# Kernel optimization log

Hardware: AMD Instinct MI355X
Metric: run time of the kernel (lower is better)

The kernel has to match this reference:

```python
import jax, jax.numpy as jnp
import numpy as np


def setup_inputs() -> dict:
    key = jax.random.key(0)
    k1, k2, k3 = jax.random.split(key, 3)
    B, T, E = 4, 2048, 1024
    x = jax.random.normal(k1, (B, T, E), dtype=jnp.float32)
    # torch nn.Linear weight layout: [out_features, in_features]
    w_qkv = jax.random.normal(k2, (3 * E, E), dtype=jnp.float32) * (E ** -0.5)
    w_out = jax.random.normal(k3, (E, E), dtype=jnp.float32) * (E ** -0.5)
    return {"x": x, "w_qkv": w_qkv, "w_out": w_out}


def reference(x, w_qkv, w_out):
    B, T, E = x.shape
    H = 16
    D = E // H  # head_dim
    # QKV projection (Linear, bias=False): x @ W.T -> [B,T,3E]
    qkv = jnp.einsum('bte,fe->btf', x, w_qkv)
    qkv = qkv.reshape(B, T, 3, H, D).transpose(2, 0, 3, 1, 4)  # [3,B,H,T,D]
    q, k, v = qkv[0], qkv[1], qkv[2]
    scale = 1.0 / jnp.sqrt(jnp.asarray(D, dtype=x.dtype))
    att = jnp.einsum('bhqd,bhkd->bhqk', q, k) * scale  # [B,H,T,T]
    causal = jnp.tril(jnp.ones((T, T), dtype=bool))
    att = jnp.where(causal[None, None], att, jnp.asarray(-jnp.inf, dtype=att.dtype))
    att = jax.nn.softmax(att, axis=-1)
    # dropout = 0.0 (eval-mode): identity
    y = jnp.einsum('bhqk,bhkd->bhqd', att, v)  # [B,H,T,D]
    y = y.transpose(0, 2, 1, 3).reshape(B, T, E)
    return jnp.einsum('bte,fe->btf', y, w_out)
```

## Files before the change

### kernel.cpp

```cpp
#include <hip/hip_runtime.h>

typedef __bf16 bf16x8 __attribute__((ext_vector_type(8)));
typedef __bf16 bf16x4 __attribute__((ext_vector_type(4)));
typedef __bf16 bf16x2 __attribute__((ext_vector_type(2)));
typedef float f32x4 __attribute__((ext_vector_type(4)));
typedef float f32x16 __attribute__((ext_vector_type(16)));
typedef unsigned short ushortx8 __attribute__((ext_vector_type(8)));
typedef unsigned short ushortx4 __attribute__((ext_vector_type(4)));
typedef unsigned int uint32x4v __attribute__((ext_vector_type(4)));

#define DEVI static __device__ __forceinline__

DEVI unsigned short f2bf(float f) {
  unsigned int u = __builtin_bit_cast(unsigned int, f);
  u += 0x7FFFu + ((u >> 16) & 1u);
  return (unsigned short)(u >> 16);
}

DEVI bf16x8 ld8(const unsigned short* p) {
  return __builtin_bit_cast(bf16x8, *(const ushortx8*)p);
}

DEVI void gll16(const unsigned short* g, unsigned short* l) {
  __builtin_amdgcn_global_load_lds((const __attribute__((address_space(1))) void*)g,
                                   (__attribute__((address_space(3))) void*)l, 16, 0, 0);
}

#define MFMA16(a, b, c) __builtin_amdgcn_mfma_f32_16x16x32_bf16(a, b, c, 0, 0, 0)
#define MFMA32(a, b, c) __builtin_amdgcn_mfma_f32_32x32x16_bf16(a, b, c, 0, 0, 0)

DEVI unsigned pkbf(float lo, float hi) {
  bf16x2 v;
  v[0] = (__bf16)lo;
  v[1] = (__bf16)hi;
  return __builtin_bit_cast(unsigned, v);
}

DEVI float swaphalf_max(float x) {
  unsigned xu = __builtin_bit_cast(unsigned, x);
  auto pr = __builtin_amdgcn_permlane32_swap(xu, xu, false, false);
  return fmaxf(__builtin_bit_cast(float, (unsigned)pr[0]),
               __builtin_bit_cast(float, (unsigned)pr[1]));
}

DEVI float swaphalf_add(float x) {
  unsigned xu = __builtin_bit_cast(unsigned, x);
  auto pr = __builtin_amdgcn_permlane32_swap(xu, xu, false, false);
  return __builtin_bit_cast(float, (unsigned)pr[0]) +
         __builtin_bit_cast(float, (unsigned)pr[1]);
}

DEVI bf16x8 ldswz(const unsigned short* L, int row, int colsh) {
  return ld8(L + row * 64 + ((((colsh * 2) ^ ((row & 7) << 4))) >> 1));
}

#define SB 4
#define ST 2048
#define SE 1024
#define SH 16
#define SD 64
#define QSCALE 0.18033688011112042f
#define DMTHR 11.541560327111708f

__global__ void cvt_f32_bf16(const float* __restrict__ in, unsigned short* __restrict__ out, int n4) {
  int i = blockIdx.x * blockDim.x + threadIdx.x;
  if (i >= n4) return;
  float4 v = ((const float4*)in)[i];
  ushortx4 o;
  o.x = f2bf(v.x); o.y = f2bf(v.y); o.z = f2bf(v.z); o.w = f2bf(v.w);
  ((ushortx4*)out)[i] = o;
}

template<int EPI>
__global__ __launch_bounds__(256, 2) void gemm_nt(
    const unsigned short* __restrict__ A, const unsigned short* __restrict__ Bw,
    float* __restrict__ Cf,
    unsigned short* __restrict__ Qo, unsigned short* __restrict__ Ko,
    unsigned short* __restrict__ VTo,
    int M, int N, int K) {
  __shared__ unsigned short As[2][128 * 64];
  __shared__ unsigned short Bs[2][128 * 64];
  const int tid = threadIdx.x;
  const int lane = tid & 63;
  const int w = tid >> 6;
  const int wr = w >> 1, wc = w & 1;
  const int r16 = lane & 15, g = lane >> 4;

  const int nwg = gridDim.x * gridDim.y;
  const int lin = blockIdx.x + blockIdx.y * gridDim.x;
  const int wg = (lin & 7) * (nwg >> 3) + (lin >> 3);
  const int bx = wg % gridDim.x, by = wg / gridDim.x;
  const int m0 = by * 128, n0 = bx * 128;

  f32x4 acc[4][4] = {};

  auto stageAB = [&](int k0, int buf) {
#pragma unroll
    for (int it = 0; it < 4; ++it) {
      int c = it * 256 + tid;
      int row = c >> 3, j = c & 7;
      int src = ((j * 16) ^ ((row & 7) << 4)) >> 1;
      gll16(A + (size_t)(m0 + row) * K + k0 + src, As[buf] + c * 8);
    }
#pragma unroll
    for (int it = 0; it < 4; ++it) {
      int c = it * 256 + tid;
      int row = c >> 3, j = c & 7;
      int src = ((j * 16) ^ ((row & 7) << 4)) >> 1;
      gll16(Bw + (size_t)(n0 + row) * K + k0 + src, Bs[buf] + c * 8);
    }
  };

  const int nt = K >> 6;
  stageAB(0, 0);
  __syncthreads();

  for (int t = 0; t < nt; ++t) {
    const int cur = t & 1;
    if (t + 1 < nt) stageAB((t + 1) << 6, cur ^ 1);

#pragma unroll
    for (int ks = 0; ks < 2; ++ks) {
      bf16x8 af[4], bfr[4];
#pragma unroll
      for (int mt = 0; mt < 4; ++mt)
        af[mt] = ldswz(As[cur], wr * 64 + mt * 16 + r16, ks * 32 + g * 8);
#pragma unroll
      for (int nt2 = 0; nt2 < 4; ++nt2)
        bfr[nt2] = ldswz(Bs[cur], wc * 64 + nt2 * 16 + r16, ks * 32 + g * 8);
#pragma unroll
      for (int mt = 0; mt < 4; ++mt)
#pragma unroll
        for (int nt2 = 0; nt2 < 4; ++nt2)
          acc[mt][nt2] = MFMA16(af[mt], bfr[nt2], acc[mt][nt2]);
    }

    __syncthreads();
  }

#pragma unroll
  for (int mt = 0; mt < 4; ++mt) {
#pragma unroll
    for (int nt2 = 0; nt2 < 4; ++nt2) {
#pragma unroll
      for (int r = 0; r < 4; ++r) {
        int m = m0 + wr * 64 + mt * 16 + g * 4 + r;
        int n = n0 + wc * 64 + nt2 * 16 + r16;
        float v = acc[mt][nt2][r];
        if (EPI == 0) {
          Cf[(size_t)m * N + n] = v;
        } else {
          int b = m >> 11, t2 = m & (ST - 1);
          int which = n >> 10, h = (n >> 6) & (SH - 1), d = n & (SD - 1);
          int bh = b * SH + h;
          if (which == 0)
            Qo[((size_t)bh * ST + t2) * SD + d] = f2bf(v * QSCALE);
          else if (which == 1)
            Ko[((size_t)bh * ST + t2) * SD + d] = f2bf(v);
          else
            VTo[((size_t)bh * SD + d) * ST + t2] = f2bf(v);
        }
      }
    }
  }
}


DEVI void stage_tile(const unsigned short* gbase, size_t rowstride,
                     unsigned short* lds, int tid) {
#pragma unroll
  for (int it = 0; it < 2; ++it) {
    int c = it * 256 + tid;
    int row = c >> 3, j = c & 7;
    int src = ((j * 16) ^ ((row & 7) << 4)) >> 1;
    gll16(gbase + (size_t)row * rowstride + src, lds + c * 8);
  }
}

__global__ __launch_bounds__(256, 4) void attn_causal(
    const unsigned short* __restrict__ Q, const unsigned short* __restrict__ Kv,
    const unsigned short* __restrict__ VT, unsigned short* __restrict__ Y) {
  __shared__ unsigned short Ks[2][64 * 64];
  __shared__ unsigned short Vs[2][64 * 64];

  const int tid = threadIdx.x;
  const int lane = tid & 63;
  const int w = tid >> 6;
  const int l5 = lane & 31, h = lane >> 5;

  const int lin = blockIdx.x + blockIdx.y * gridDim.x;
  const int xcd = lin & 7;
  const int idx = lin >> 3;
  const int qt = (ST / 128 - 1) - (idx >> 3);
  const int bh = xcd + 8 * (idx & 7);
  const size_t base = (size_t)bh * ST * SD;

  const int q_glob = qt * 128 + w * 32 + l5;
  const int qwmin = qt * 128 + w * 32;

  bf16x8 qf[4];
#pragma unroll
  for (int kk = 0; kk < 4; ++kk)
    qf[kk] = ld8(Q + base + (size_t)q_glob * SD + kk * 16 + h * 8);

  float mrow = -__builtin_inff();
  float lrow = 0.f;
  f32x16 acc[2] = {};

  const int nkv = 2 * qt + 2;
  stage_tile(Kv + base, SD, Ks[0], tid);
  stage_tile(VT + base, ST, Vs[0], tid);
  __syncthreads();

  for (int kvt = 0; kvt < nkv; ++kvt) {
    const int cur = kvt & 1;
    if (kvt + 1 < nkv) {
      stage_tile(Kv + base + (size_t)(kvt + 1) * 64 * SD, SD, Ks[cur ^ 1], tid);
      stage_tile(VT + base + (kvt + 1) * 64, ST, Vs[cur ^ 1], tid);
    }

    const bool active = (kvt * 64) <= (qwmin + 31);
    if (active) {
      f32x16 s0 = {}, s1 = {};
      __builtin_amdgcn_s_setprio(1);
#pragma unroll
      for (int kk = 0; kk < 4; ++kk) {
        bf16x8 k0 = ldswz(Ks[cur], l5, kk * 16 + h * 8);
        s0 = MFMA32(k0, qf[kk], s0);
      }
#pragma unroll
      for (int kk = 0; kk < 4; ++kk) {
        bf16x8 k1 = ldswz(Ks[cur], 32 + l5, kk * 16 + h * 8);
        s1 = MFMA32(k1, qf[kk], s1);
      }
      __builtin_amdgcn_s_setprio(0);

      if (kvt * 64 + 63 > qwmin) {
        const int t0 = kvt * 64 + 4 * h;
#pragma unroll
        for (int reg = 0; reg < 16; ++reg) {
          int t = t0 + (reg & 3) + 8 * (reg >> 2);
          if (t > q_glob) s0[reg] = -__builtin_inff();
          if (t + 32 > q_glob) s1[reg] = -__builtin_inff();
        }
      }

      f32x16 mx;
#pragma unroll
      for (int i = 0; i < 16; ++i) mx[i] = fmaxf(s0[i], s1[i]);
#pragma unroll
      for (int i = 0; i < 8; ++i) mx[i] = fmaxf(mx[i], mx[i + 8]);
#pragma unroll
      for (int i = 0; i < 4; ++i) mx[i] = fmaxf(mx[i], mx[i + 4]);
      float bm = fmaxf(fmaxf(mx[0], mx[1]), fmaxf(mx[2], mx[3]));
      bm = swaphalf_max(bm);

      if (__any(bm > mrow + DMTHR)) {
        float mn = fmaxf(mrow, bm);
        float corr = exp2f(mrow - mn);
        mrow = mn;
        lrow *= corr;
#pragma unroll
        for (int dblk = 0; dblk < 2; ++dblk)
#pragma unroll
          for (int i = 0; i < 16; ++i) acc[dblk][i] *= corr;
      }

#pragma unroll
      for (int i = 0; i < 16; ++i) {
        s0[i] = exp2f(s0[i] - mrow);
        s1[i] = exp2f(s1[i] - mrow);
      }
      f32x16 sm;
#pragma unroll
      for (int i = 0; i < 16; ++i) sm[i] = s0[i] + s1[i];
#pragma unroll
      for (int i = 0; i < 8; ++i) sm[i] += sm[i + 8];
#pragma unroll
      for (int i = 0; i < 4; ++i) sm[i] += sm[i + 4];
      float rs = (sm[0] + sm[1]) + (sm[2] + sm[3]);
      lrow += swaphalf_add(rs);

      bf16x8 pb[2][2];
      auto packblk = [&](const f32x16& S, bf16x8* out) {
        unsigned a = pkbf(S[0], S[1]), b2 = pkbf(S[2], S[3]);
        unsigned c = pkbf(S[4], S[5]), d2 = pkbf(S[6], S[7]);
        auto r0 = __builtin_amdgcn_permlane32_swap(a, c, false, false);
        auto r1 = __builtin_amdgcn_permlane32_swap(b2, d2, false, false);
        uint32x4v w0 = {(unsigned)r0[0], (unsigned)r1[0], (unsigned)r0[1], (unsigned)r1[1]};
        out[0] = __builtin_bit_cast(bf16x8, w0);
        unsigned e = pkbf(S[8], S[9]), f2 = pkbf(S[10], S[11]);
        unsigned g2 = pkbf(S[12], S[13]), h2 = pkbf(S[14], S[15]);
        auto r2 = __builtin_amdgcn_permlane32_swap(e, g2, false, false);
        auto r3 = __builtin_amdgcn_permlane32_swap(f2, h2, false, false);
        uint32x4v w1 = {(unsigned)r2[0], (unsigned)r3[0], (unsigned)r2[1], (unsigned)r3[1]};
        out[1] = __builtin_bit_cast(bf16x8, w1);
      };
      packblk(s0, pb[0]);
      packblk(s1, pb[1]);

      __builtin_amdgcn_s_setprio(1);
#pragma unroll
      for (int dblk = 0; dblk < 2; ++dblk)
#pragma unroll
        for (int tt = 0; tt < 2; ++tt)
#pragma unroll
          for (int sl = 0; sl < 2; ++sl) {
            bf16x8 va = ldswz(Vs[cur], dblk * 32 + l5, tt * 32 + sl * 16 + h * 8);
            acc[dblk] = MFMA32(va, pb[tt][sl], acc[dblk]);
          }
      __builtin_amdgcn_s_setprio(0);
    }

    __syncthreads();
  }

  const int b = bh >> 4, hd = bh & 15;
  const float inv = 1.f / lrow;
#pragma unroll
  for (int dblk = 0; dblk < 2; ++dblk)
#pragma unroll
    for (int rg = 0; rg < 4; ++rg) {
      bf16x4 o;
#pragma unroll
      for (int j = 0; j < 4; ++j) o[j] = (__bf16)(acc[dblk][rg * 4 + j] * inv);
      int d = dblk * 32 + rg * 8 + 4 * h;
      *(ushortx4*)&Y[((size_t)b * ST + q_glob) * SE + hd * SD + d] =
          __builtin_bit_cast(ushortx4, o);
    }
}

extern "C" void kernel_launch(void* const* d_in, const int* in_sizes, int n_in,
                              void* d_out, int out_size, void* d_ws, size_t ws_size,
                              hipStream_t stream) {
  const float* x = (const float*)d_in[0];
  const float* w_qkv = (const float*)d_in[1];
  const float* w_out = (const float*)d_in[2];
  float* out = (float*)d_out;

  const size_t NX = (size_t)SB * ST * SE;
  const size_t NQKV = (size_t)3 * SE * SE;
  const size_t NWO = (size_t)SE * SE;
  const size_t NHD = (size_t)SB * SH * ST * SD;

  unsigned short* xb    = (unsigned short*)d_ws;
  unsigned short* wqkvb = xb + NX;
  unsigned short* woutb = wqkvb + NQKV;
  unsigned short* q     = woutb + NWO;
  unsigned short* k     = q + NHD;
  unsigned short* vT    = k + NHD;
  unsigned short* y     = xb;

  cvt_f32_bf16<<<(int)(NX / 4 + 255) / 256, 256, 0, stream>>>(x, xb, (int)(NX / 4));
  cvt_f32_bf16<<<(int)(NQKV / 4 + 255) / 256, 256, 0, stream>>>(w_qkv, wqkvb, (int)(NQKV / 4));
  cvt_f32_bf16<<<(int)(NWO / 4 + 255) / 256, 256, 0, stream>>>(w_out, woutb, (int)(NWO / 4));

  gemm_nt<1><<<dim3(3 * SE / 128, SB * ST / 128), 256, 0, stream>>>(
      xb, wqkvb, nullptr, q, k, vT, SB * ST, 3 * SE, SE);

  attn_causal<<<dim3(ST / 128, SB * SH), 256, 0, stream>>>(q, k, vT, y);

  gemm_nt<0><<<dim3(SE / 128, SB * ST / 128), 256, 0, stream>>>(
      y, woutb, out, nullptr, nullptr, nullptr, SB * ST, SE, SE);
}
```

Measured before the change: 199.2 us.

## Use 128x256 GEMM tiles with 8 waves and a triple-buffered interleaved pipeline

The NT GEMM now uses a 128x256 output tile computed by 512 threads (8 waves). Staging moves to a three-deep LDS ring that prefetches two K-steps ahead. Each K-step is split into four MFMA phases, with one global-to-LDS staging unit issued between phases. Explicit vmcnt waits, barriers and s_setprio raise MFMA priority and overlap loads with compute. The cost is larger LDS use (about 144KB), which likely limits occupancy to one block per CU.

```diff
diff --git a/kernel.cpp b/kernel.cpp
--- a/kernel.cpp
+++ b/kernel.cpp
@@ -71,71 +71,118 @@
   ((ushortx4*)out)[i] = o;
 }
 
+
+DEVI void stage_unit(const unsigned short* gsrc, int K,
+                     unsigned short* ldst, int tid) {
+#pragma unroll
+  for (int it = 0; it < 2; ++it) {
+    int c = it * 512 + tid;
+    int row = c >> 3, j = c & 7;
+    int src = ((j * 16) ^ ((row & 7) << 4)) >> 1;
+    gll16(gsrc + (size_t)row * K + src, ldst + c * 8);
+  }
+}
+
 template<int EPI>
-__global__ __launch_bounds__(256, 2) void gemm_nt(
+__global__ __launch_bounds__(512, 2) void gemm_nt(
     const unsigned short* __restrict__ A, const unsigned short* __restrict__ Bw,
     float* __restrict__ Cf,
     unsigned short* __restrict__ Qo, unsigned short* __restrict__ Ko,
     unsigned short* __restrict__ VTo,
     int M, int N, int K) {
-  __shared__ unsigned short As[2][128 * 64];
-  __shared__ unsigned short Bs[2][128 * 64];
+  __shared__ unsigned short As[3][128 * 64];
+  __shared__ unsigned short Bs[3][256 * 64];
   const int tid = threadIdx.x;
   const int lane = tid & 63;
   const int w = tid >> 6;
-  const int wr = w >> 1, wc = w & 1;
+  const int wc = w >> 1, wr = w & 1;
   const int r16 = lane & 15, g = lane >> 4;
 
   const int nwg = gridDim.x * gridDim.y;
   const int lin = blockIdx.x + blockIdx.y * gridDim.x;
   const int wg = (lin & 7) * (nwg >> 3) + (lin >> 3);
   const int bx = wg % gridDim.x, by = wg / gridDim.x;
-  const int m0 = by * 128, n0 = bx * 128;
+  const int m0 = by * 128, n0 = bx * 256;
+
+  const unsigned short* Abase = A + (size_t)m0 * K;
+  const unsigned short* Bbase0 = Bw + (size_t)n0 * K;
+  const unsigned short* Bbase1 = Bw + (size_t)(n0 + 128) * K;
 
   f32x4 acc[4][4] = {};
 
-  auto stageAB = [&](int k0, int buf) {
-#pragma unroll
-    for (int it = 0; it < 4; ++it) {
-      int c = it * 256 + tid;
-      int row = c >> 3, j = c & 7;
-      int src = ((j * 16) ^ ((row & 7) << 4)) >> 1;
-      gll16(A + (size_t)(m0 + row) * K + k0 + src, As[buf] + c * 8);
-    }
-#pragma unroll
-    for (int it = 0; it < 4; ++it) {
-      int c = it * 256 + tid;
-      int row = c >> 3, j = c & 7;
-      int src = ((j * 16) ^ ((row & 7) << 4)) >> 1;
-      gll16(Bw + (size_t)(n0 + row) * K + k0 + src, Bs[buf] + c * 8);
-    }
-  };
-
-  const int nt = K >> 6;
-  stageAB(0, 0);
-  __syncthreads();
-
-  for (int t = 0; t < nt; ++t) {
-    const int cur = t & 1;
-    if (t + 1 < nt) stageAB((t + 1) << 6, cur ^ 1);
-
-#pragma unroll
-    for (int ks = 0; ks < 2; ++ks) {
-      bf16x8 af[4], bfr[4];
-#pragma unroll
-      for (int mt = 0; mt < 4; ++mt)
-        af[mt] = ldswz(As[cur], wr * 64 + mt * 16 + r16, ks * 32 + g * 8);
-#pragma unroll
-      for (int nt2 = 0; nt2 < 4; ++nt2)
-        bfr[nt2] = ldswz(Bs[cur], wc * 64 + nt2 * 16 + r16, ks * 32 + g * 8);
-#pragma unroll
-      for (int mt = 0; mt < 4; ++mt)
-#pragma unroll
-        for (int nt2 = 0; nt2 < 4; ++nt2)
-          acc[mt][nt2] = MFMA16(af[mt], bfr[nt2], acc[mt][nt2]);
-    }
-
-    __syncthreads();
+  const int ntk = K >> 6;
+#pragma unroll
+  for (int t = 0; t < 2; ++t) {
+    stage_unit(Abase + (t << 6), K, As[t], tid);
+    stage_unit(Bbase0 + (t << 6), K, Bs[t], tid);
+    stage_unit(Bbase1 + (t << 6), K, Bs[t] + 128 * 64, tid);
+  }
+  asm volatile("s_waitcnt vmcnt(6)" ::: "memory");
+  __builtin_amdgcn_s_barrier();
+  __builtin_amdgcn_sched_barrier(0);
+
+  int cur = 0;
+  for (int t = 0; t < ntk; ++t) {
+    int nb = cur + 2; if (nb >= 3) nb -= 3;
+    const unsigned short* Ab = As[cur];
+    const unsigned short* Bb = Bs[cur];
+    const bool pf = (t + 2 < ntk);
+    const int k2 = (t + 2) << 6;
+
+    bf16x8 af[4], bfr[2];
+
+    if (pf) stage_unit(Abase + k2, K, As[nb], tid);
+#pragma unroll
+    for (int m = 0; m < 4; ++m) af[m] = ldswz(Ab, wr * 64 + m * 16 + r16, g * 8);
+#pragma unroll
+    for (int n = 0; n < 2; ++n) bfr[n] = ldswz(Bb, wc * 64 + n * 16 + r16, g * 8);
+    __builtin_amdgcn_s_setprio(1);
+#pragma unroll
+    for (int m = 0; m < 4; ++m)
+#pragma unroll
+      for (int n = 0; n < 2; ++n) acc[m][n] = MFMA16(af[m], bfr[n], acc[m][n]);
+    __builtin_amdgcn_s_setprio(0);
+    __builtin_amdgcn_s_barrier();
+
+    if (pf) stage_unit(Bbase0 + k2, K, Bs[nb], tid);
+#pragma unroll
+    for (int n = 0; n < 2; ++n) bfr[n] = ldswz(Bb, wc * 64 + (2 + n) * 16 + r16, g * 8);
+    __builtin_amdgcn_s_setprio(1);
+#pragma unroll
+    for (int m = 0; m < 4; ++m)
+#pragma unroll
+      for (int n = 0; n < 2; ++n) acc[m][2 + n] = MFMA16(af[m], bfr[n], acc[m][2 + n]);
+    __builtin_amdgcn_s_setprio(0);
+    __builtin_amdgcn_s_barrier();
+
+    if (pf) stage_unit(Bbase1 + k2, K, Bs[nb] + 128 * 64, tid);
+#pragma unroll
+    for (int m = 0; m < 4; ++m) af[m] = ldswz(Ab, wr * 64 + m * 16 + r16, 32 + g * 8);
+#pragma unroll
+    for (int n = 0; n < 2; ++n) bfr[n] = ldswz(Bb, wc * 64 + n * 16 + r16, 32 + g * 8);
+    __builtin_amdgcn_s_setprio(1);
+#pragma unroll
+    for (int m = 0; m < 4; ++m)
+#pragma unroll
+      for (int n = 0; n < 2; ++n) acc[m][n] = MFMA16(af[m], bfr[n], acc[m][n]);
+    __builtin_amdgcn_s_setprio(0);
+    __builtin_amdgcn_s_barrier();
+
+#pragma unroll
+    for (int n = 0; n < 2; ++n) bfr[n] = ldswz(Bb, wc * 64 + (2 + n) * 16 + r16, 32 + g * 8);
+    __builtin_amdgcn_s_setprio(1);
+#pragma unroll
+    for (int m = 0; m < 4; ++m)
+#pragma unroll
+      for (int n = 0; n < 2; ++n) acc[m][2 + n] = MFMA16(af[m], bfr[n], acc[m][2 + n]);
+    __builtin_amdgcn_s_setprio(0);
+
+    if (pf) asm volatile("s_waitcnt vmcnt(6)" ::: "memory");
+    else    asm volatile("s_waitcnt vmcnt(0)" ::: "memory");
+    __builtin_amdgcn_s_barrier();
+    __builtin_amdgcn_sched_barrier(0);
+
+    cur = (cur == 2) ? 0 : cur + 1;
   }
 
 #pragma unroll
@@ -355,11 +402,11 @@
   cvt_f32_bf16<<<(int)(NQKV / 4 + 255) / 256, 256, 0, stream>>>(w_qkv, wqkvb, (int)(NQKV / 4));
   cvt_f32_bf16<<<(int)(NWO / 4 + 255) / 256, 256, 0, stream>>>(w_out, woutb, (int)(NWO / 4));
 
-  gemm_nt<1><<<dim3(3 * SE / 128, SB * ST / 128), 256, 0, stream>>>(
+  gemm_nt<1><<<dim3(3 * SE / 256, SB * ST / 128), 512, 0, stream>>>(
       xb, wqkvb, nullptr, q, k, vT, SB * ST, 3 * SE, SE);
 
   attn_causal<<<dim3(ST / 128, SB * SH), 256, 0, stream>>>(q, k, vT, y);
 
-  gemm_nt<0><<<dim3(SE / 128, SB * ST / 128), 256, 0, stream>>>(
+  gemm_nt<0><<<dim3(SE / 256, SB * ST / 128), 512, 0, stream>>>(
       y, woutb, out, nullptr, nullptr, nullptr, SB * ST, SE, SE);
 }
```

Result: slower. 246.1 us (+23.5%).
